# Optimization experiments

Measured on AMD Instinct MI355X. Metric: run time of the kernel, lower is better.

Reference implementation:

```python
import jax, jax.numpy as jnp
import numpy as np
from jax import lax

B, C, HH, WW = 256, 2048, 24, 8
NC = 51
KM_ITERS = 10
EPS = 1e-5


def _bn(x, g, b, m, v):
    return (x - m) / jnp.sqrt(v + EPS) * g + b


def _kmeans_ids(X):
    # X: [C, D]. Cluster the C channel vectors into 4 groups (Lloyd's, euclidean,
    # deterministic quartile init standing in for kmeans-pytorch random init).
    Cn = X.shape[0]
    centers = X[jnp.array([0, Cn // 4, Cn // 2, 3 * Cn // 4])]  # [4, D]
    xs = jnp.sum(X * X, axis=1)  # [C]

    def d2(cent):  # squared euclidean distances [C, 4]
        return xs[:, None] - 2.0 * (X @ cent.T) + jnp.sum(cent * cent, axis=1)[None]

    def step(cent, _):
        ids = jnp.argmin(d2(cent), axis=1)
        oh = jax.nn.one_hot(ids, 4, dtype=X.dtype)  # [C, 4]
        cnt = oh.sum(0)[:, None]  # [4, 1]
        new = jnp.where(cnt > 0, (oh.T @ X) / jnp.maximum(cnt, 1.0), cent)
        return new, None

    centers, _ = lax.scan(step, centers, None, length=KM_ITERS)
    return jnp.argmin(d2(centers), axis=1)  # [C]


def setup_inputs() -> dict:
    key = jax.random.key(0)
    ks = iter(jax.random.split(key, 64))
    rn = lambda shape, s=1.0: jax.random.normal(next(ks), shape, jnp.float32) * s
    ru = lambda shape: jax.random.uniform(next(ks), shape, jnp.float32, minval=0.5, maxval=1.5)
    return dict(
        x=rn((B, C, HH, WW)),
        Wg=rn((512, 2048), 0.02), bg=rn((512,), 0.02),
        g_gamma=ru((512,)), g_beta=rn((512,), 0.1), g_mean=rn((512,), 0.1), g_var=ru((512,)),
        gb_gamma=ru((512,)), gb_beta=rn((512,), 0.1), gb_mean=rn((512,), 0.1), gb_var=ru((512,)),
        Wcg=rn((NC, 512), 0.01), bcg=jnp.zeros((NC,), jnp.float32),
        W1=rn((512, 2048), 0.02), b1=rn((512,), 0.02),
        n1_gamma=ru((512,)), n1_beta=rn((512,), 0.1), n1_mean=rn((512,), 0.1), n1_var=ru((512,)),
        W2=rn((128, 512), 0.05), b2=rn((128,), 0.02),
        n2_gamma=ru((128,)), n2_beta=rn((128,), 0.1), n2_mean=rn((128,), 0.1), n2_var=ru((128,)),
        bk_gamma=ru((4, 128)), bk_beta=rn((4, 128), 0.1), bk_mean=rn((4, 128), 0.1), bk_var=ru((4, 128)),
        Wck=rn((NC, 512), 0.01), bck=jnp.zeros((NC,), jnp.float32),
    )


def reference(x, Wg, bg, g_gamma, g_beta, g_mean, g_var,
              gb_gamma, gb_beta, gb_mean, gb_var, Wcg, bcg,
              W1, b1, n1_gamma, n1_beta, n1_mean, n1_var,
              W2, b2, n2_gamma, n2_beta, n2_mean, n2_var,
              bk_gamma, bk_beta, bk_mean, bk_var, Wck, bck):
    b_, c_ = x.shape[0], x.shape[1]
    pooled = x.mean(axis=(2, 3))  # [B, C] (adaptive avgpool to 1x1)

    # ---- global branch: 1x1 conv on pooled == dense layer ----
    xg = jax.nn.relu(_bn(pooled @ Wg.T + bg, g_gamma, g_beta, g_mean, g_var))
    xg = _bn(xg, gb_gamma, gb_beta, gb_mean, gb_var)  # bottleneck_global
    x_prelogits = xg @ Wcg.T + bcg  # [B, NC]

    # ---- kmeans branch ----
    X = x.reshape(b_, c_, -1)  # per-sample [C, H*W]
    ids = jax.vmap(_kmeans_ids)(lax.stop_gradient(X))  # [B, C] int32
    masks = jax.nn.one_hot(ids, 4, dtype=x.dtype)  # [B, C, 4]
    # masking zeroes whole channels, so avgpool(masked map) == masked pooled
    Pk = jnp.einsum('bc,bck->kbc', pooled, masks)  # [4, B, C]

    # NOTE: original forward reuses norm_kmeans1 weights for all 4 branches
    h = jax.nn.relu(_bn(jnp.einsum('kbc,oc->kbo', Pk, W1) + b1,
                        n1_gamma, n1_beta, n1_mean, n1_var))  # [4, B, 512]
    h = jax.nn.relu(_bn(jnp.einsum('kbo,po->kbp', h, W2) + b2,
                        n2_gamma, n2_beta, n2_mean, n2_var))  # [4, B, 128]
    # per-branch bottleneck BN1d (stacked params [4, 128])
    h = (h - bk_mean[:, None, :]) / jnp.sqrt(bk_var[:, None, :] + EPS) \
        * bk_gamma[:, None, :] + bk_beta[:, None, :]
    # triple-nested copy loop == concat [x1|x2|x3|x4] along features
    y = jnp.transpose(h, (1, 0, 2)).reshape(b_, -1)  # [B, 512]
    y_prelogits = y @ Wck.T + bck  # [B, NC]

    return (x_prelogits, y_prelogits)
```

## Files before the change

kernel.cpp:

```cpp
#include <hip/hip_runtime.h>
#include <math.h>

#define B_   256
#define C_   2048
#define D_   192
#define EPSf 1e-5f
#define BLAS_Q 384

__device__ __forceinline__ float pw96_sq_f4(const float4* a4) {
    float r0 = 0.f, r1 = 0.f, r2 = 0.f, r3 = 0.f, r4 = 0.f, r5 = 0.f, r6 = 0.f, r7 = 0.f;
#pragma unroll
    for (int i = 0; i < 12; ++i) {
        const float4 v0 = a4[2 * i], v1 = a4[2 * i + 1];
        r0 += __fmul_rn(v0.x, v0.x); r1 += __fmul_rn(v0.y, v0.y);
        r2 += __fmul_rn(v0.z, v0.z); r3 += __fmul_rn(v0.w, v0.w);
        r4 += __fmul_rn(v1.x, v1.x); r5 += __fmul_rn(v1.y, v1.y);
        r6 += __fmul_rn(v1.z, v1.z); r7 += __fmul_rn(v1.w, v1.w);
    }
    return ((r0 + r1) + (r2 + r3)) + ((r4 + r5) + (r6 + r7));
}

__device__ __forceinline__ float pw96_sq_s(const float* a) {
    float r0 = 0.f, r1 = 0.f, r2 = 0.f, r3 = 0.f, r4 = 0.f, r5 = 0.f, r6 = 0.f, r7 = 0.f;
#pragma unroll
    for (int i = 0; i < 12; ++i) {
        r0 += __fmul_rn(a[8 * i + 0], a[8 * i + 0]);
        r1 += __fmul_rn(a[8 * i + 1], a[8 * i + 1]);
        r2 += __fmul_rn(a[8 * i + 2], a[8 * i + 2]);
        r3 += __fmul_rn(a[8 * i + 3], a[8 * i + 3]);
        r4 += __fmul_rn(a[8 * i + 4], a[8 * i + 4]);
        r5 += __fmul_rn(a[8 * i + 5], a[8 * i + 5]);
        r6 += __fmul_rn(a[8 * i + 6], a[8 * i + 6]);
        r7 += __fmul_rn(a[8 * i + 7], a[8 * i + 7]);
    }
    return ((r0 + r1) + (r2 + r3)) + ((r4 + r5) + (r6 + r7));
}

__global__ __launch_bounds__(256) void transpose_kernel(const float* __restrict__ x,
                                                        float* __restrict__ xT) {
    const int b = blockIdx.z, c0 = blockIdx.x * 64, d0 = blockIdx.y * 64;
    const float* X = x + (size_t)b * (C_ * (size_t)D_);
    float* XT      = xT + (size_t)b * (C_ * (size_t)D_);
    __shared__ float tile[64][65];
    const int tx = threadIdx.x & 63, ty = threadIdx.x >> 6;
#pragma unroll
    for (int i = 0; i < 16; ++i) {
        const int c = ty + i * 4;
        tile[c][tx] = X[(size_t)(c0 + c) * D_ + d0 + tx];
    }
    __syncthreads();
#pragma unroll
    for (int i = 0; i < 16; ++i) {
        const int d = ty + i * 4;
        XT[(size_t)(d0 + d) * C_ + c0 + tx] = tile[tx][d];
    }
}

__global__ __launch_bounds__(512) void kmeans_fast_kernel(const float* __restrict__ x,
                                                          const float* __restrict__ xT,
                                                          float* __restrict__ pooled,
                                                          unsigned char* __restrict__ ids_out) {
    const int b = blockIdx.x, t = threadIdx.x;
    const int lane = t & 63;
    const float* X   = x  + (size_t)b * (C_ * (size_t)D_);
    const float* XTb = xT + (size_t)b * (C_ * (size_t)D_);

    __shared__ __align__(16) float cent[4][192];
    __shared__ float xs_s[C_];
    __shared__ float part[6][4][192];
    __shared__ float cs4[4];
    __shared__ int   cnt[4];
    __shared__ int   changed;
    __shared__ unsigned char ids[C_];

    if (t < 192) {
        cent[0][t] = X[(size_t)0    * D_ + t];
        cent[1][t] = X[(size_t)512  * D_ + t];
        cent[2][t] = X[(size_t)1024 * D_ + t];
        cent[3][t] = X[(size_t)1536 * D_ + t];
    }

    {
        const float4* pA = (const float4*)XTb + t;
        float sq0 = 0.f, sq1 = 0.f, sq2 = 0.f, sq3 = 0.f;
        float sm0 = 0.f, sm1 = 0.f, sm2 = 0.f, sm3 = 0.f;
#pragma unroll
        for (int blk = 0; blk < 2; ++blk) {
            float q[4][8], s[4][8];
#pragma unroll
            for (int ch = 0; ch < 4; ++ch)
#pragma unroll
                for (int j = 0; j < 8; ++j) { q[ch][j] = 0.f; s[ch][j] = 0.f; }
            for (int i = 0; i < 12; ++i) {
                float4 vb[8];
#pragma unroll
                for (int u = 0; u < 8; ++u) vb[u] = pA[(blk * 96 + 8 * i + u) << 9];
#pragma unroll
                for (int u = 0; u < 8; ++u) {
                    q[0][u] += __fmul_rn(vb[u].x, vb[u].x); s[0][u] += vb[u].x;
                    q[1][u] += __fmul_rn(vb[u].y, vb[u].y); s[1][u] += vb[u].y;
                    q[2][u] += __fmul_rn(vb[u].z, vb[u].z); s[2][u] += vb[u].z;
                    q[3][u] += __fmul_rn(vb[u].w, vb[u].w); s[3][u] += vb[u].w;
                }
            }
            sq0 += ((q[0][0] + q[0][1]) + (q[0][2] + q[0][3])) + ((q[0][4] + q[0][5]) + (q[0][6] + q[0][7]));
            sq1 += ((q[1][0] + q[1][1]) + (q[1][2] + q[1][3])) + ((q[1][4] + q[1][5]) + (q[1][6] + q[1][7]));
            sq2 += ((q[2][0] + q[2][1]) + (q[2][2] + q[2][3])) + ((q[2][4] + q[2][5]) + (q[2][6] + q[2][7]));
            sq3 += ((q[3][0] + q[3][1]) + (q[3][2] + q[3][3])) + ((q[3][4] + q[3][5]) + (q[3][6] + q[3][7]));
            sm0 += ((s[0][0] + s[0][1]) + (s[0][2] + s[0][3])) + ((s[0][4] + s[0][5]) + (s[0][6] + s[0][7]));
            sm1 += ((s[1][0] + s[1][1]) + (s[1][2] + s[1][3])) + ((s[1][4] + s[1][5]) + (s[1][6] + s[1][7]));
            sm2 += ((s[2][0] + s[2][1]) + (s[2][2] + s[2][3])) + ((s[2][4] + s[2][5]) + (s[2][6] + s[2][7]));
            sm3 += ((s[3][0] + s[3][1]) + (s[3][2] + s[3][3])) + ((s[3][4] + s[3][5]) + (s[3][6] + s[3][7]));
        }
        xs_s[4 * t + 0] = sq0; xs_s[4 * t + 1] = sq1;
        xs_s[4 * t + 2] = sq2; xs_s[4 * t + 3] = sq3;
        *(float4*)(pooled + (size_t)b * C_ + 4 * t) =
            make_float4(sm0 / 192.0f, sm1 / 192.0f, sm2 / 192.0f, sm3 / 192.0f);
        ids[4 * t + 0] = 255; ids[4 * t + 1] = 255;
        ids[4 * t + 2] = 255; ids[4 * t + 3] = 255;
    }
    __syncthreads();

    for (int iter = 0;; ++iter) {
        if (t < 4) {
            cs4[t] = pw96_sq_s(cent[t]) + pw96_sq_s(cent[t] + 96);
            cnt[t] = 0;
        }
        if (t == 0) changed = 0;
        __syncthreads();

        const float q0 = cs4[0], q1 = cs4[1], q2 = cs4[2], q3 = cs4[3];

        int lc0 = 0, lc1 = 0, lc2 = 0, lc3 = 0, mych = 0;
        {
            const float4* pA = (const float4*)XTb + t;
            float acc[4][4] = {};
            for (int db = 0; db < 192; db += 8) {
                float4 vb[8];
#pragma unroll
                for (int u = 0; u < 8; ++u) vb[u] = pA[(db + u) << 9];
#pragma unroll
                for (int u = 0; u < 8; ++u) {
                    const int d = db + u;
                    const float c0 = cent[0][d], c1 = cent[1][d];
                    const float c2 = cent[2][d], c3 = cent[3][d];
                    acc[0][0] = fmaf(vb[u].x, c0, acc[0][0]);
                    acc[1][0] = fmaf(vb[u].y, c0, acc[1][0]);
                    acc[2][0] = fmaf(vb[u].z, c0, acc[2][0]);
                    acc[3][0] = fmaf(vb[u].w, c0, acc[3][0]);
                    acc[0][1] = fmaf(vb[u].x, c1, acc[0][1]);
                    acc[1][1] = fmaf(vb[u].y, c1, acc[1][1]);
                    acc[2][1] = fmaf(vb[u].z, c1, acc[2][1]);
                    acc[3][1] = fmaf(vb[u].w, c1, acc[3][1]);
                    acc[0][2] = fmaf(vb[u].x, c2, acc[0][2]);
                    acc[1][2] = fmaf(vb[u].y, c2, acc[1][2]);
                    acc[2][2] = fmaf(vb[u].z, c2, acc[2][2]);
                    acc[3][2] = fmaf(vb[u].w, c2, acc[3][2]);
                    acc[0][3] = fmaf(vb[u].x, c3, acc[0][3]);
                    acc[1][3] = fmaf(vb[u].y, c3, acc[1][3]);
                    acc[2][3] = fmaf(vb[u].z, c3, acc[2][3]);
                    acc[3][3] = fmaf(vb[u].w, c3, acc[3][3]);
                }
            }
#pragma unroll
            for (int ch = 0; ch < 4; ++ch) {
                const int c = 4 * t + ch;
                const float xv = xs_s[c];
                const float e0 = (xv - 2.0f * acc[ch][0]) + q0;
                const float e1 = (xv - 2.0f * acc[ch][1]) + q1;
                const float e2 = (xv - 2.0f * acc[ch][2]) + q2;
                const float e3 = (xv - 2.0f * acc[ch][3]) + q3;
                int id = 0; float best = e0;
                if (e1 < best) { best = e1; id = 1; }
                if (e2 < best) { best = e2; id = 2; }
                if (e3 < best) { best = e3; id = 3; }
                lc0 += (id == 0); lc1 += (id == 1); lc2 += (id == 2); lc3 += (id == 3);
                mych |= (ids[c] != (unsigned char)id);
                ids[c] = (unsigned char)id;
            }
        }
#pragma unroll
        for (int off = 32; off > 0; off >>= 1) {
            lc0 += __shfl_down(lc0, off);
            lc1 += __shfl_down(lc1, off);
            lc2 += __shfl_down(lc2, off);
            lc3 += __shfl_down(lc3, off);
        }
        if (lane == 0) {
            atomicAdd(&cnt[0], lc0); atomicAdd(&cnt[1], lc1);
            atomicAdd(&cnt[2], lc2); atomicAdd(&cnt[3], lc3);
        }
        if (mych) changed = 1;
        __syncthreads();

        if (changed == 0 || iter == 10) break;

        if (t < 288) {
            const int kb = t / 48;
            const int dg = t - kb * 48;
            const int cb = kb * BLAS_Q;
            const int ce = (cb + BLAS_Q < C_) ? (cb + BLAS_Q) : C_;
            const float4* pB = (const float4*)X + (size_t)cb * 48 + dg;
            float s[4][4] = {};
            for (int c0i = 0; c0i < ce - cb; c0i += 8) {
                float4 vb[8];
#pragma unroll
                for (int u = 0; u < 8; ++u) vb[u] = pB[(size_t)(c0i + u) * 48];
#pragma unroll
                for (int u = 0; u < 8; ++u) {
                    const int id = ids[cb + c0i + u];
                    s[0][0] += (id == 0) ? vb[u].x : 0.0f;
                    s[1][0] += (id == 0) ? vb[u].y : 0.0f;
                    s[2][0] += (id == 0) ? vb[u].z : 0.0f;
                    s[3][0] += (id == 0) ? vb[u].w : 0.0f;
                    s[0][1] += (id == 1) ? vb[u].x : 0.0f;
                    s[1][1] += (id == 1) ? vb[u].y : 0.0f;
                    s[2][1] += (id == 1) ? vb[u].z : 0.0f;
                    s[3][1] += (id == 1) ? vb[u].w : 0.0f;
                    s[0][2] += (id == 2) ? vb[u].x : 0.0f;
                    s[1][2] += (id == 2) ? vb[u].y : 0.0f;
                    s[2][2] += (id == 2) ? vb[u].z : 0.0f;
                    s[3][2] += (id == 2) ? vb[u].w : 0.0f;
                    s[0][3] += (id == 3) ? vb[u].x : 0.0f;
                    s[1][3] += (id == 3) ? vb[u].y : 0.0f;
                    s[2][3] += (id == 3) ? vb[u].z : 0.0f;
                    s[3][3] += (id == 3) ? vb[u].w : 0.0f;
                }
            }
#pragma unroll
            for (int k = 0; k < 4; ++k) {
                part[kb][k][4 * dg + 0] = s[0][k];
                part[kb][k][4 * dg + 1] = s[1][k];
                part[kb][k][4 * dg + 2] = s[2][k];
                part[kb][k][4 * dg + 3] = s[3][k];
            }
        }
        __syncthreads();
        if (t < 192) {
#pragma unroll
            for (int k = 0; k < 4; ++k) {
                float tt = part[0][k][t];
                tt += part[1][k][t];
                tt += part[2][k][t];
                tt += part[3][k][t];
                tt += part[4][k][t];
                tt += part[5][k][t];
                if (cnt[k] > 0) cent[k][t] = tt / (float)cnt[k];
            }
        }
        __syncthreads();
    }

    *(uchar4*)(ids_out + (size_t)b * C_ + 4 * t) = *(uchar4*)&ids[4 * t];
}

__global__ __launch_bounds__(256) void pool_kernel(const float* __restrict__ x,
                                                   float* __restrict__ pooled) {
    const int row  = blockIdx.x * 4 + (threadIdx.x >> 6);
    const int lane = threadIdx.x & 63;
    const float* r = x + (size_t)row * D_;
    float s = 0.f;
    if (lane < 48) {
        const float4 v = ((const float4*)r)[lane];
        s = v.x + v.y + v.z + v.w;
    }
#pragma unroll
    for (int off = 32; off > 0; off >>= 1) s += __shfl_down(s, off);
    if (lane == 0) pooled[row] = s * (1.f / 192.f);
}

__global__ __launch_bounds__(512) void kmeans_fb_kernel(const float* __restrict__ x,
                                                        unsigned char* __restrict__ ids_out) {
    const int b = blockIdx.x, t = threadIdx.x;
    const int lane = t & 63;
    const float* X = x + (size_t)b * (C_ * (size_t)D_);

    __shared__ __align__(16) float cent[4][192];
    __shared__ float xs_s[C_];
    __shared__ float cs4[4];
    __shared__ int   cnt[4];
    __shared__ int   changed;
    __shared__ unsigned char ids[C_];

    if (t < 192) {
        cent[0][t] = X[(size_t)0    * D_ + t];
        cent[1][t] = X[(size_t)512  * D_ + t];
        cent[2][t] = X[(size_t)1024 * D_ + t];
        cent[3][t] = X[(size_t)1536 * D_ + t];
    }
    for (int c = t; c < C_; c += 512) {
        const float4* r4 = (const float4*)(X + (size_t)c * D_);
        xs_s[c] = pw96_sq_f4(r4) + pw96_sq_f4(r4 + 24);
        ids[c]  = 255;
    }
    __syncthreads();

    for (int iter = 0;; ++iter) {
        if (t < 4) {
            cs4[t] = pw96_sq_s(cent[t]) + pw96_sq_s(cent[t] + 96);
            cnt[t] = 0;
        }
        if (t == 0) changed = 0;
        __syncthreads();

        const float q0 = cs4[0], q1 = cs4[1], q2 = cs4[2], q3 = cs4[3];
        int lc0 = 0, lc1 = 0, lc2 = 0, lc3 = 0, mych = 0;
        for (int j = 0; j < 4; ++j) {
            const int c = t + 512 * j;
            const float4* r4 = (const float4*)(X + (size_t)c * D_);
            float d0 = 0.f, d1 = 0.f, d2 = 0.f, d3 = 0.f;
#pragma unroll 8
            for (int i = 0; i < 48; ++i) {
                const float4 a  = r4[i];
                const float4 c0 = *(const float4*)&cent[0][4 * i];
                const float4 c1 = *(const float4*)&cent[1][4 * i];
                const float4 c2 = *(const float4*)&cent[2][4 * i];
                const float4 c3 = *(const float4*)&cent[3][4 * i];
                d0 = fmaf(a.x, c0.x, d0); d0 = fmaf(a.y, c0.y, d0);
                d0 = fmaf(a.z, c0.z, d0); d0 = fmaf(a.w, c0.w, d0);
                d1 = fmaf(a.x, c1.x, d1); d1 = fmaf(a.y, c1.y, d1);
                d1 = fmaf(a.z, c1.z, d1); d1 = fmaf(a.w, c1.w, d1);
                d2 = fmaf(a.x, c2.x, d2); d2 = fmaf(a.y, c2.y, d2);
                d2 = fmaf(a.z, c2.z, d2); d2 = fmaf(a.w, c2.w, d2);
                d3 = fmaf(a.x, c3.x, d3); d3 = fmaf(a.y, c3.y, d3);
                d3 = fmaf(a.z, c3.z, d3); d3 = fmaf(a.w, c3.w, d3);
            }
            const float xv = xs_s[c];
            const float e0 = (xv - 2.0f * d0) + q0;
            const float e1 = (xv - 2.0f * d1) + q1;
            const float e2 = (xv - 2.0f * d2) + q2;
            const float e3 = (xv - 2.0f * d3) + q3;
            int id = 0; float best = e0;
            if (e1 < best) { best = e1; id = 1; }
            if (e2 < best) { best = e2; id = 2; }
            if (e3 < best) { best = e3; id = 3; }
            lc0 += (id == 0); lc1 += (id == 1); lc2 += (id == 2); lc3 += (id == 3);
            mych |= (ids[c] != (unsigned char)id);
            ids[c] = (unsigned char)id;
        }
#pragma unroll
        for (int off = 32; off > 0; off >>= 1) {
            lc0 += __shfl_down(lc0, off);
            lc1 += __shfl_down(lc1, off);
            lc2 += __shfl_down(lc2, off);
            lc3 += __shfl_down(lc3, off);
        }
        if (lane == 0) {
            atomicAdd(&cnt[0], lc0); atomicAdd(&cnt[1], lc1);
            atomicAdd(&cnt[2], lc2); atomicAdd(&cnt[3], lc3);
        }
        if (mych) changed = 1;
        __syncthreads();

        if (changed == 0 || iter == 10) break;

        if (t < 192) {
            float t0 = 0.f, t1 = 0.f, t2 = 0.f, t3 = 0.f;
            for (int kb = 0; kb < C_; kb += BLAS_Q) {
                const int ke = (kb + BLAS_Q < C_) ? (kb + BLAS_Q) : C_;
                float s0 = 0.f, s1 = 0.f, s2 = 0.f, s3 = 0.f;
                for (int c = kb; c < ke; ++c) {
                    const float xv = X[(size_t)c * D_ + t];
                    const int id = ids[c];
                    s0 += (id == 0) ? xv : 0.0f;
                    s1 += (id == 1) ? xv : 0.0f;
                    s2 += (id == 2) ? xv : 0.0f;
                    s3 += (id == 3) ? xv : 0.0f;
                }
                t0 += s0; t1 += s1; t2 += s2; t3 += s3;
            }
            if (cnt[0] > 0) cent[0][t] = t0 / (float)cnt[0];
            if (cnt[1] > 0) cent[1][t] = t1 / (float)cnt[1];
            if (cnt[2] > 0) cent[2][t] = t2 / (float)cnt[2];
            if (cnt[3] > 0) cent[3][t] = t3 / (float)cnt[3];
        }
        __syncthreads();
    }

    for (int c = t; c < C_; c += 512) ids_out[(size_t)b * C_ + c] = ids[c];
}

__device__ __forceinline__ float bn_apply(float v, float g, float be, float m, float va) {
    return (v - m) / sqrtf(va + EPSf) * g + be;
}

__global__ __launch_bounds__(256) void gemm1_kernel(
    const float* __restrict__ pooled, const unsigned char* __restrict__ ids,
    const float* __restrict__ Wg, const float* __restrict__ bg,
    const float* __restrict__ g_gamma, const float* __restrict__ g_beta,
    const float* __restrict__ g_mean, const float* __restrict__ g_var,
    const float* __restrict__ gb_gamma, const float* __restrict__ gb_beta,
    const float* __restrict__ gb_mean, const float* __restrict__ gb_var,
    const float* __restrict__ W1, const float* __restrict__ b1,
    const float* __restrict__ n1_gamma, const float* __restrict__ n1_beta,
    const float* __restrict__ n1_mean, const float* __restrict__ n1_var,
    float* __restrict__ xg2, float* __restrict__ h1) {
    const int z = blockIdx.z;
    const int bn0 = blockIdx.x * 64, bm0 = blockIdx.y * 64;
    const float* Bmat = (z == 0) ? Wg : W1;
    __shared__ float As[32][68];
    __shared__ float Bs[32][68];
    float acc[4][4] = {};
    const int t = threadIdx.x;
    const int tx = t & 15, ty = t >> 4;

    for (int k0 = 0; k0 < 2048; k0 += 32) {
#pragma unroll
        for (int u = 0; u < 2; ++u) {
            const int idx = t + 256 * u;
            const int m = idx >> 3, kc = idx & 7;
            float4 v = *(const float4*)(pooled + (size_t)(bm0 + m) * 2048 + k0 + kc * 4);
            if (z > 0) {
                const unsigned int uu =
                    *(const unsigned int*)(ids + (size_t)(bm0 + m) * 2048 + k0 + kc * 4);
                const unsigned int k = (unsigned int)(z - 1);
                v.x = ((uu & 0xffu) == k) ? v.x : 0.f;
                v.y = (((uu >> 8) & 0xffu) == k) ? v.y : 0.f;
                v.z = (((uu >> 16) & 0xffu) == k) ? v.z : 0.f;
                v.w = (((uu >> 24) & 0xffu) == k) ? v.w : 0.f;
            }
            As[kc * 4 + 0][m] = v.x; As[kc * 4 + 1][m] = v.y;
            As[kc * 4 + 2][m] = v.z; As[kc * 4 + 3][m] = v.w;
            const float4 wv = *(const float4*)(Bmat + (size_t)(bn0 + m) * 2048 + k0 + kc * 4);
            Bs[kc * 4 + 0][m] = wv.x; Bs[kc * 4 + 1][m] = wv.y;
            Bs[kc * 4 + 2][m] = wv.z; Bs[kc * 4 + 3][m] = wv.w;
        }
        __syncthreads();
#pragma unroll 8
        for (int kk = 0; kk < 32; ++kk) {
            const float4 a = *(const float4*)&As[kk][ty * 4];
            const float4 wv = *(const float4*)&Bs[kk][tx * 4];
            const float av[4] = {a.x, a.y, a.z, a.w};
            const float bv[4] = {wv.x, wv.y, wv.z, wv.w};
#pragma unroll
            for (int i = 0; i < 4; ++i)
#pragma unroll
                for (int j = 0; j < 4; ++j) acc[i][j] += av[i] * bv[j];
        }
        __syncthreads();
    }

    const int m0 = bm0 + ty * 4, n0 = bn0 + tx * 4;
    if (z == 0) {
#pragma unroll
        for (int j = 0; j < 4; ++j) {
            const int n = n0 + j;
            const float bgv = bg[n];
            const float g1 = g_gamma[n], be1 = g_beta[n], mm1 = g_mean[n], vv1 = g_var[n];
            const float g2 = gb_gamma[n], be2 = gb_beta[n], mm2 = gb_mean[n], vv2 = gb_var[n];
#pragma unroll
            for (int i = 0; i < 4; ++i) {
                float v = acc[i][j] + bgv;
                v = bn_apply(v, g1, be1, mm1, vv1);
                v = fmaxf(v, 0.f);
                v = bn_apply(v, g2, be2, mm2, vv2);
                xg2[(size_t)(m0 + i) * 512 + n] = v;
            }
        }
    } else {
        const int k = z - 1;
#pragma unroll
        for (int j = 0; j < 4; ++j) {
            const int n = n0 + j;
            const float b1v = b1[n];
            const float g1 = n1_gamma[n], be1 = n1_beta[n], mm1 = n1_mean[n], vv1 = n1_var[n];
#pragma unroll
            for (int i = 0; i < 4; ++i) {
                float v = acc[i][j] + b1v;
                v = bn_apply(v, g1, be1, mm1, vv1);
                v = fmaxf(v, 0.f);
                h1[((size_t)k * 256 + (m0 + i)) * 512 + n] = v;
            }
        }
    }
}

__global__ __launch_bounds__(256) void gemm2_kernel(
    const float* __restrict__ h1, const float* __restrict__ W2,
    const float* __restrict__ b2,
    const float* __restrict__ n2_gamma, const float* __restrict__ n2_beta,
    const float* __restrict__ n2_mean, const float* __restrict__ n2_var,
    const float* __restrict__ bk_gamma, const float* __restrict__ bk_beta,
    const float* __restrict__ bk_mean, const float* __restrict__ bk_var,
    float* __restrict__ yv) {
    const int bn0 = blockIdx.x * 64, bm0 = blockIdx.y * 64;
    __shared__ float As[32][68];
    __shared__ float Bs[32][68];
    float acc[4][4] = {};
    const int t = threadIdx.x;
    const int tx = t & 15, ty = t >> 4;

    for (int k0 = 0; k0 < 512; k0 += 32) {
#pragma unroll
        for (int u = 0; u < 2; ++u) {
            const int idx = t + 256 * u;
            const int m = idx >> 3, kc = idx & 7;
            const float4 v = *(const float4*)(h1 + (size_t)(bm0 + m) * 512 + k0 + kc * 4);
            As[kc * 4 + 0][m] = v.x; As[kc * 4 + 1][m] = v.y;
            As[kc * 4 + 2][m] = v.z; As[kc * 4 + 3][m] = v.w;
            const float4 wv = *(const float4*)(W2 + (size_t)(bn0 + m) * 512 + k0 + kc * 4);
            Bs[kc * 4 + 0][m] = wv.x; Bs[kc * 4 + 1][m] = wv.y;
            Bs[kc * 4 + 2][m] = wv.z; Bs[kc * 4 + 3][m] = wv.w;
        }
        __syncthreads();
#pragma unroll 8
        for (int kk = 0; kk < 32; ++kk) {
            const float4 a = *(const float4*)&As[kk][ty * 4];
            const float4 wv = *(const float4*)&Bs[kk][tx * 4];
            const float av[4] = {a.x, a.y, a.z, a.w};
            const float bv[4] = {wv.x, wv.y, wv.z, wv.w};
#pragma unroll
            for (int i = 0; i < 4; ++i)
#pragma unroll
                for (int j = 0; j < 4; ++j) acc[i][j] += av[i] * bv[j];
        }
        __syncthreads();
    }

    const int m0 = bm0 + ty * 4, n0 = bn0 + tx * 4;
#pragma unroll
    for (int j = 0; j < 4; ++j) {
        const int n = n0 + j;
        const float b2v = b2[n];
        const float g1 = n2_gamma[n], be1 = n2_beta[n], mm1 = n2_mean[n], vv1 = n2_var[n];
#pragma unroll
        for (int i = 0; i < 4; ++i) {
            const int row = m0 + i;
            const int k = row >> 8, b = row & 255;
            float v = acc[i][j] + b2v;
            v = bn_apply(v, g1, be1, mm1, vv1);
            v = fmaxf(v, 0.f);
            const int pi = k * 128 + n;
            v = bn_apply(v, bk_gamma[pi], bk_beta[pi], bk_mean[pi], bk_var[pi]);
            yv[(size_t)b * 512 + pi] = v;
        }
    }
}

__global__ __launch_bounds__(128) void head_kernel(
    const float* __restrict__ xg2, const float* __restrict__ yv,
    const float* __restrict__ Wcg, const float* __restrict__ bcg,
    const float* __restrict__ Wck, const float* __restrict__ bck,
    float* __restrict__ out) {
    const int b = blockIdx.x, t = threadIdx.x;
    __shared__ float xr[512], yr[512];
    ((float4*)xr)[t] = ((const float4*)(xg2 + (size_t)b * 512))[t];
    ((float4*)yr)[t] = ((const float4*)(yv + (size_t)b * 512))[t];
    __syncthreads();
    if (t < 51) {
        float acc = 0.f;
        const float4* wr = (const float4*)(Wcg + (size_t)t * 512);
        const float4* xv = (const float4*)xr;
#pragma unroll 8
        for (int p = 0; p < 128; ++p) {
            const float4 w4 = wr[p], v4 = xv[p];
            acc += w4.x * v4.x + w4.y * v4.y + w4.z * v4.z + w4.w * v4.w;
        }
        out[(size_t)b * 51 + t] = acc + bcg[t];
    } else if (t >= 64 && t < 115) {
        const int n = t - 64;
        float acc = 0.f;
        const float4* wr = (const float4*)(Wck + (size_t)n * 512);
        const float4* yv4 = (const float4*)yr;
#pragma unroll 8
        for (int p = 0; p < 128; ++p) {
            const float4 w4 = wr[p], v4 = yv4[p];
            acc += w4.x * v4.x + w4.y * v4.y + w4.z * v4.z + w4.w * v4.w;
        }
        out[(size_t)(B_ * 51) + (size_t)b * 51 + n] = acc + bck[n];
    }
}

extern "C" void kernel_launch(void* const* d_in, const int* in_sizes, int n_in,
                              void* d_out, int out_size, void* d_ws, size_t ws_size,
                              hipStream_t stream) {
    const float* x        = (const float*)d_in[0];
    const float* Wg       = (const float*)d_in[1];
    const float* bg       = (const float*)d_in[2];
    const float* g_gamma  = (const float*)d_in[3];
    const float* g_beta   = (const float*)d_in[4];
    const float* g_mean   = (const float*)d_in[5];
    const float* g_var    = (const float*)d_in[6];
    const float* gb_gamma = (const float*)d_in[7];
    const float* gb_beta  = (const float*)d_in[8];
    const float* gb_mean  = (const float*)d_in[9];
    const float* gb_var   = (const float*)d_in[10];
    const float* Wcg      = (const float*)d_in[11];
    const float* bcg      = (const float*)d_in[12];
    const float* W1       = (const float*)d_in[13];
    const float* b1       = (const float*)d_in[14];
    const float* n1_gamma = (const float*)d_in[15];
    const float* n1_beta  = (const float*)d_in[16];
    const float* n1_mean  = (const float*)d_in[17];
    const float* n1_var   = (const float*)d_in[18];
    const float* W2       = (const float*)d_in[19];
    const float* b2       = (const float*)d_in[20];
    const float* n2_gamma = (const float*)d_in[21];
    const float* n2_beta  = (const float*)d_in[22];
    const float* n2_mean  = (const float*)d_in[23];
    const float* n2_var   = (const float*)d_in[24];
    const float* bk_gamma = (const float*)d_in[25];
    const float* bk_beta  = (const float*)d_in[26];
    const float* bk_mean  = (const float*)d_in[27];
    const float* bk_var   = (const float*)d_in[28];
    const float* Wck      = (const float*)d_in[29];
    const float* bck      = (const float*)d_in[30];
    float* out = (float*)d_out;

    const size_t xt_elems    = (size_t)B_ * C_ * D_;
    const size_t small_elems = 524288 + 131072 + 524288 + 131072;
    const size_t need_fast   = xt_elems * 4 + small_elems * 4 + 524288 + 256;

    if (ws_size >= need_fast) {
        float* xT          = (float*)d_ws;
        float* pooled      = xT + xt_elems;
        unsigned char* ids = (unsigned char*)(pooled + 524288);
        float* xg2         = (float*)(ids + 524288);
        float* h1          = xg2 + 131072;
        float* yv          = h1 + 524288;

        transpose_kernel<<<dim3(32, 3, B_), dim3(256), 0, stream>>>(x, xT);
        kmeans_fast_kernel<<<dim3(B_), dim3(512), 0, stream>>>(x, xT, pooled, ids);
        gemm1_kernel<<<dim3(8, 4, 5), dim3(256), 0, stream>>>(
            pooled, ids, Wg, bg, g_gamma, g_beta, g_mean, g_var,
            gb_gamma, gb_beta, gb_mean, gb_var, W1, b1,
            n1_gamma, n1_beta, n1_mean, n1_var, xg2, h1);
        gemm2_kernel<<<dim3(2, 16), dim3(256), 0, stream>>>(
            h1, W2, b2, n2_gamma, n2_beta, n2_mean, n2_var,
            bk_gamma, bk_beta, bk_mean, bk_var, yv);
        head_kernel<<<dim3(B_), dim3(128), 0, stream>>>(xg2, yv, Wcg, bcg, Wck, bck, out);
    } else {
        float* pooled      = (float*)d_ws;
        unsigned char* ids = (unsigned char*)(pooled + 524288);
        float* xg2         = (float*)(ids + 524288);
        float* h1          = xg2 + 131072;
        float* yv          = h1 + 524288;

        pool_kernel<<<dim3((B_ * C_) / 4), dim3(256), 0, stream>>>(x, pooled);
        kmeans_fb_kernel<<<dim3(B_), dim3(512), 0, stream>>>(x, ids);
        gemm1_kernel<<<dim3(8, 4, 5), dim3(256), 0, stream>>>(
            pooled, ids, Wg, bg, g_gamma, g_beta, g_mean, g_var,
            gb_gamma, gb_beta, gb_mean, gb_var, W1, b1,
            n1_gamma, n1_beta, n1_mean, n1_var, xg2, h1);
        gemm2_kernel<<<dim3(2, 16), dim3(256), 0, stream>>>(
            h1, W2, b2, n2_gamma, n2_beta, n2_mean, n2_var,
            bk_gamma, bk_beta, bk_mean, bk_var, yv);
        head_kernel<<<dim3(B_), dim3(128), 0, stream>>>(xg2, yv, Wcg, bcg, Wck, bck, out);
    }
}
```

Measured before the change: 1.791 ms.

## Fuse pooling and norms into transpose, double kmeans block to 1024 threads

The transpose kernel now loads a full 64-channel row tile into LDS, computes per-channel squared norms and pooled means there, and writes the transposed data. This removes the separate norm/pool pass from the kmeans kernel. The kmeans kernel moves to 1024 threads with two channels per thread and float2 loads, double-buffered in both the distance and centroid-accumulation phases, to raise parallelism and hide memory latency. The cost is more LDS in the transpose (64x193 floats, lowering its occupancy), an extra xs buffer in global memory, and fewer registers available per thread at 1024 threads.

```diff
diff --git a/kernel.cpp b/kernel.cpp
--- a/kernel.cpp
+++ b/kernel.cpp
@@ -36,30 +36,92 @@
     return ((r0 + r1) + (r2 + r3)) + ((r4 + r5) + (r6 + r7));
 }
 
+__device__ __forceinline__ float pw96_sum_s(const float* a) {
+    float r0 = 0.f, r1 = 0.f, r2 = 0.f, r3 = 0.f, r4 = 0.f, r5 = 0.f, r6 = 0.f, r7 = 0.f;
+#pragma unroll
+    for (int i = 0; i < 12; ++i) {
+        r0 += a[8 * i + 0]; r1 += a[8 * i + 1];
+        r2 += a[8 * i + 2]; r3 += a[8 * i + 3];
+        r4 += a[8 * i + 4]; r5 += a[8 * i + 5];
+        r6 += a[8 * i + 6]; r7 += a[8 * i + 7];
+    }
+    return ((r0 + r1) + (r2 + r3)) + ((r4 + r5) + (r6 + r7));
+}
+
 __global__ __launch_bounds__(256) void transpose_kernel(const float* __restrict__ x,
-                                                        float* __restrict__ xT) {
-    const int b = blockIdx.z, c0 = blockIdx.x * 64, d0 = blockIdx.y * 64;
+                                                        float* __restrict__ xT,
+                                                        float* __restrict__ pooled,
+                                                        float* __restrict__ xs_g) {
+    const int c0 = blockIdx.x * 64, b = blockIdx.y;
     const float* X = x + (size_t)b * (C_ * (size_t)D_);
     float* XT      = xT + (size_t)b * (C_ * (size_t)D_);
-    __shared__ float tile[64][65];
-    const int tx = threadIdx.x & 63, ty = threadIdx.x >> 6;
-#pragma unroll
-    for (int i = 0; i < 16; ++i) {
-        const int c = ty + i * 4;
-        tile[c][tx] = X[(size_t)(c0 + c) * D_ + d0 + tx];
+    __shared__ float lds[64 * 193];
+    const int t = threadIdx.x;
+
+#pragma unroll
+    for (int i = 0; i < 12; ++i) {
+        const int idx = i * 256 + t;
+        const int r = idx / 48, j = idx % 48;
+        const float4 v = *(const float4*)(X + (size_t)(c0 + r) * D_ + 4 * j);
+        float* p = &lds[r * 193 + 4 * j];
+        p[0] = v.x; p[1] = v.y; p[2] = v.z; p[3] = v.w;
     }
     __syncthreads();
-#pragma unroll
-    for (int i = 0; i < 16; ++i) {
-        const int d = ty + i * 4;
-        XT[(size_t)(d0 + d) * C_ + c0 + tx] = tile[tx][d];
-    }
-}
-
-__global__ __launch_bounds__(512) void kmeans_fast_kernel(const float* __restrict__ x,
-                                                          const float* __restrict__ xT,
-                                                          float* __restrict__ pooled,
-                                                          unsigned char* __restrict__ ids_out) {
+
+    if (t < 64) {
+        const float* row = &lds[t * 193];
+        xs_g[(size_t)b * C_ + c0 + t]   = pw96_sq_s(row)  + pw96_sq_s(row + 96);
+        pooled[(size_t)b * C_ + c0 + t] = (pw96_sum_s(row) + pw96_sum_s(row + 96)) / 192.0f;
+    }
+
+#pragma unroll
+    for (int i = 0; i < 48; ++i) {
+        const int idx = i * 256 + t;
+        const int d = idx >> 6, ch = idx & 63;
+        XT[(size_t)d * C_ + c0 + ch] = lds[ch * 193 + d];
+    }
+}
+
+__device__ __forceinline__ void pa_comp8_f2(const float2 (&vb)[8], int dbase,
+                                            const float (*cent)[192],
+                                            float (&acc)[2][4]) {
+#pragma unroll
+    for (int u = 0; u < 8; ++u) {
+        const int d = dbase + u;
+        const float c0 = cent[0][d], c1 = cent[1][d];
+        const float c2 = cent[2][d], c3 = cent[3][d];
+        acc[0][0] = fmaf(vb[u].x, c0, acc[0][0]);
+        acc[1][0] = fmaf(vb[u].y, c0, acc[1][0]);
+        acc[0][1] = fmaf(vb[u].x, c1, acc[0][1]);
+        acc[1][1] = fmaf(vb[u].y, c1, acc[1][1]);
+        acc[0][2] = fmaf(vb[u].x, c2, acc[0][2]);
+        acc[1][2] = fmaf(vb[u].y, c2, acc[1][2]);
+        acc[0][3] = fmaf(vb[u].x, c3, acc[0][3]);
+        acc[1][3] = fmaf(vb[u].y, c3, acc[1][3]);
+    }
+}
+
+__device__ __forceinline__ void pb_comp8_f2(const float2 (&vb)[8], int cbase,
+                                            const unsigned char* ids,
+                                            float (&s)[2][4]) {
+#pragma unroll
+    for (int u = 0; u < 8; ++u) {
+        const int id = ids[cbase + u];
+        s[0][0] += (id == 0) ? vb[u].x : 0.0f;
+        s[1][0] += (id == 0) ? vb[u].y : 0.0f;
+        s[0][1] += (id == 1) ? vb[u].x : 0.0f;
+        s[1][1] += (id == 1) ? vb[u].y : 0.0f;
+        s[0][2] += (id == 2) ? vb[u].x : 0.0f;
+        s[1][2] += (id == 2) ? vb[u].y : 0.0f;
+        s[0][3] += (id == 3) ? vb[u].x : 0.0f;
+        s[1][3] += (id == 3) ? vb[u].y : 0.0f;
+    }
+}
+
+__global__ __launch_bounds__(1024) void kmeans_fast_kernel(const float* __restrict__ x,
+                                                           const float* __restrict__ xT,
+                                                           const float* __restrict__ xs_g,
+                                                           unsigned char* __restrict__ ids_out) {
     const int b = blockIdx.x, t = threadIdx.x;
     const int lane = t & 63;
     const float* X   = x  + (size_t)b * (C_ * (size_t)D_);
@@ -79,45 +141,11 @@
         cent[2][t] = X[(size_t)1024 * D_ + t];
         cent[3][t] = X[(size_t)1536 * D_ + t];
     }
-
     {
-        const float4* pA = (const float4*)XTb + t;
-        float sq0 = 0.f, sq1 = 0.f, sq2 = 0.f, sq3 = 0.f;
-        float sm0 = 0.f, sm1 = 0.f, sm2 = 0.f, sm3 = 0.f;
-#pragma unroll
-        for (int blk = 0; blk < 2; ++blk) {
-            float q[4][8], s[4][8];
-#pragma unroll
-            for (int ch = 0; ch < 4; ++ch)
-#pragma unroll
-                for (int j = 0; j < 8; ++j) { q[ch][j] = 0.f; s[ch][j] = 0.f; }
-            for (int i = 0; i < 12; ++i) {
-                float4 vb[8];
-#pragma unroll
-                for (int u = 0; u < 8; ++u) vb[u] = pA[(blk * 96 + 8 * i + u) << 9];
-#pragma unroll
-                for (int u = 0; u < 8; ++u) {
-                    q[0][u] += __fmul_rn(vb[u].x, vb[u].x); s[0][u] += vb[u].x;
-                    q[1][u] += __fmul_rn(vb[u].y, vb[u].y); s[1][u] += vb[u].y;
-                    q[2][u] += __fmul_rn(vb[u].z, vb[u].z); s[2][u] += vb[u].z;
-                    q[3][u] += __fmul_rn(vb[u].w, vb[u].w); s[3][u] += vb[u].w;
-                }
-            }
-            sq0 += ((q[0][0] + q[0][1]) + (q[0][2] + q[0][3])) + ((q[0][4] + q[0][5]) + (q[0][6] + q[0][7]));
-            sq1 += ((q[1][0] + q[1][1]) + (q[1][2] + q[1][3])) + ((q[1][4] + q[1][5]) + (q[1][6] + q[1][7]));
-            sq2 += ((q[2][0] + q[2][1]) + (q[2][2] + q[2][3])) + ((q[2][4] + q[2][5]) + (q[2][6] + q[2][7]));
-            sq3 += ((q[3][0] + q[3][1]) + (q[3][2] + q[3][3])) + ((q[3][4] + q[3][5]) + (q[3][6] + q[3][7]));
-            sm0 += ((s[0][0] + s[0][1]) + (s[0][2] + s[0][3])) + ((s[0][4] + s[0][5]) + (s[0][6] + s[0][7]));
-            sm1 += ((s[1][0] + s[1][1]) + (s[1][2] + s[1][3])) + ((s[1][4] + s[1][5]) + (s[1][6] + s[1][7]));
-            sm2 += ((s[2][0] + s[2][1]) + (s[2][2] + s[2][3])) + ((s[2][4] + s[2][5]) + (s[2][6] + s[2][7]));
-            sm3 += ((s[3][0] + s[3][1]) + (s[3][2] + s[3][3])) + ((s[3][4] + s[3][5]) + (s[3][6] + s[3][7]));
-        }
-        xs_s[4 * t + 0] = sq0; xs_s[4 * t + 1] = sq1;
-        xs_s[4 * t + 2] = sq2; xs_s[4 * t + 3] = sq3;
-        *(float4*)(pooled + (size_t)b * C_ + 4 * t) =
-            make_float4(sm0 / 192.0f, sm1 / 192.0f, sm2 / 192.0f, sm3 / 192.0f);
-        ids[4 * t + 0] = 255; ids[4 * t + 1] = 255;
-        ids[4 * t + 2] = 255; ids[4 * t + 3] = 255;
+        const int c2 = 2 * t;
+        const float2 xv2 = *(const float2*)(xs_g + (size_t)b * C_ + c2);
+        xs_s[c2] = xv2.x; xs_s[c2 + 1] = xv2.y;
+        ids[c2] = 255; ids[c2 + 1] = 255;
     }
     __syncthreads();
 
@@ -133,38 +161,24 @@
 
         int lc0 = 0, lc1 = 0, lc2 = 0, lc3 = 0, mych = 0;
         {
-            const float4* pA = (const float4*)XTb + t;
-            float acc[4][4] = {};
-            for (int db = 0; db < 192; db += 8) {
-                float4 vb[8];
-#pragma unroll
-                for (int u = 0; u < 8; ++u) vb[u] = pA[(db + u) << 9];
-#pragma unroll
-                for (int u = 0; u < 8; ++u) {
-                    const int d = db + u;
-                    const float c0 = cent[0][d], c1 = cent[1][d];
-                    const float c2 = cent[2][d], c3 = cent[3][d];
-                    acc[0][0] = fmaf(vb[u].x, c0, acc[0][0]);
-                    acc[1][0] = fmaf(vb[u].y, c0, acc[1][0]);
-                    acc[2][0] = fmaf(vb[u].z, c0, acc[2][0]);
-                    acc[3][0] = fmaf(vb[u].w, c0, acc[3][0]);
-                    acc[0][1] = fmaf(vb[u].x, c1, acc[0][1]);
-                    acc[1][1] = fmaf(vb[u].y, c1, acc[1][1]);
-                    acc[2][1] = fmaf(vb[u].z, c1, acc[2][1]);
-                    acc[3][1] = fmaf(vb[u].w, c1, acc[3][1]);
-                    acc[0][2] = fmaf(vb[u].x, c2, acc[0][2]);
-                    acc[1][2] = fmaf(vb[u].y, c2, acc[1][2]);
-                    acc[2][2] = fmaf(vb[u].z, c2, acc[2][2]);
-                    acc[3][2] = fmaf(vb[u].w, c2, acc[3][2]);
-                    acc[0][3] = fmaf(vb[u].x, c3, acc[0][3]);
-                    acc[1][3] = fmaf(vb[u].y, c3, acc[1][3]);
-                    acc[2][3] = fmaf(vb[u].z, c3, acc[2][3]);
-                    acc[3][3] = fmaf(vb[u].w, c3, acc[3][3]);
+            const float2* pA = (const float2*)XTb + t;
+            float acc[2][4] = {};
+            float2 bufA[8], bufB[8];
+#pragma unroll
+            for (int u = 0; u < 8; ++u) bufA[u] = pA[(size_t)u << 10];
+            for (int db = 0; db < 192; db += 16) {
+#pragma unroll
+                for (int u = 0; u < 8; ++u) bufB[u] = pA[(size_t)(db + 8 + u) << 10];
+                pa_comp8_f2(bufA, db, cent, acc);
+                if (db + 16 < 192) {
+#pragma unroll
+                    for (int u = 0; u < 8; ++u) bufA[u] = pA[(size_t)(db + 16 + u) << 10];
                 }
-            }
-#pragma unroll
-            for (int ch = 0; ch < 4; ++ch) {
-                const int c = 4 * t + ch;
+                pa_comp8_f2(bufB, db + 8, cent, acc);
+            }
+#pragma unroll
+            for (int ch = 0; ch < 2; ++ch) {
+                const int c = 2 * t + ch;
                 const float xv = xs_s[c];
                 const float e0 = (xv - 2.0f * acc[ch][0]) + q0;
                 const float e1 = (xv - 2.0f * acc[ch][1]) + q1;
@@ -195,44 +209,31 @@
 
         if (changed == 0 || iter == 10) break;
 
-        if (t < 288) {
-            const int kb = t / 48;
-            const int dg = t - kb * 48;
+        if (t < 576) {
+            const int kb = t / 96;
+            const int dg = t - kb * 96;
             const int cb = kb * BLAS_Q;
             const int ce = (cb + BLAS_Q < C_) ? (cb + BLAS_Q) : C_;
-            const float4* pB = (const float4*)X + (size_t)cb * 48 + dg;
-            float s[4][4] = {};
-            for (int c0i = 0; c0i < ce - cb; c0i += 8) {
-                float4 vb[8];
-#pragma unroll
-                for (int u = 0; u < 8; ++u) vb[u] = pB[(size_t)(c0i + u) * 48];
-#pragma unroll
-                for (int u = 0; u < 8; ++u) {
-                    const int id = ids[cb + c0i + u];
-                    s[0][0] += (id == 0) ? vb[u].x : 0.0f;
-                    s[1][0] += (id == 0) ? vb[u].y : 0.0f;
-                    s[2][0] += (id == 0) ? vb[u].z : 0.0f;
-                    s[3][0] += (id == 0) ? vb[u].w : 0.0f;
-                    s[0][1] += (id == 1) ? vb[u].x : 0.0f;
-                    s[1][1] += (id == 1) ? vb[u].y : 0.0f;
-                    s[2][1] += (id == 1) ? vb[u].z : 0.0f;
-                    s[3][1] += (id == 1) ? vb[u].w : 0.0f;
-                    s[0][2] += (id == 2) ? vb[u].x : 0.0f;
-                    s[1][2] += (id == 2) ? vb[u].y : 0.0f;
-                    s[2][2] += (id == 2) ? vb[u].z : 0.0f;
-                    s[3][2] += (id == 2) ? vb[u].w : 0.0f;
-                    s[0][3] += (id == 3) ? vb[u].x : 0.0f;
-                    s[1][3] += (id == 3) ? vb[u].y : 0.0f;
-                    s[2][3] += (id == 3) ? vb[u].z : 0.0f;
-                    s[3][3] += (id == 3) ? vb[u].w : 0.0f;
+            const int nb = (ce - cb) >> 3;
+            const float2* pB = (const float2*)X + (size_t)cb * 96 + dg;
+            float s[2][4] = {};
+            float2 bufA[8], bufB[8];
+#pragma unroll
+            for (int u = 0; u < 8; ++u) bufA[u] = pB[(size_t)u * 96];
+            for (int ib = 0; ib < nb; ib += 2) {
+#pragma unroll
+                for (int u = 0; u < 8; ++u) bufB[u] = pB[(size_t)((ib + 1) * 8 + u) * 96];
+                pb_comp8_f2(bufA, cb + ib * 8, ids, s);
+                if (ib + 2 < nb) {
+#pragma unroll
+                    for (int u = 0; u < 8; ++u) bufA[u] = pB[(size_t)((ib + 2) * 8 + u) * 96];
                 }
+                pb_comp8_f2(bufB, cb + (ib + 1) * 8, ids, s);
             }
 #pragma unroll
             for (int k = 0; k < 4; ++k) {
-                part[kb][k][4 * dg + 0] = s[0][k];
-                part[kb][k][4 * dg + 1] = s[1][k];
-                part[kb][k][4 * dg + 2] = s[2][k];
-                part[kb][k][4 * dg + 3] = s[3][k];
+                part[kb][k][2 * dg + 0] = s[0][k];
+                part[kb][k][2 * dg + 1] = s[1][k];
             }
         }
         __syncthreads();
@@ -251,7 +252,7 @@
         __syncthreads();
     }
 
-    *(uchar4*)(ids_out + (size_t)b * C_ + 4 * t) = *(uchar4*)&ids[4 * t];
+    *(uchar2*)(ids_out + (size_t)b * C_ + 2 * t) = *(uchar2*)&ids[2 * t];
 }
 
 __global__ __launch_bounds__(256) void pool_kernel(const float* __restrict__ x,
@@ -608,19 +609,20 @@
     float* out = (float*)d_out;
 
     const size_t xt_elems    = (size_t)B_ * C_ * D_;
-    const size_t small_elems = 524288 + 131072 + 524288 + 131072;
+    const size_t small_elems = 524288 * 2 + 131072 + 524288 + 131072;
     const size_t need_fast   = xt_elems * 4 + small_elems * 4 + 524288 + 256;
 
     if (ws_size >= need_fast) {
         float* xT          = (float*)d_ws;
         float* pooled      = xT + xt_elems;
-        unsigned char* ids = (unsigned char*)(pooled + 524288);
+        float* xs_g        = pooled + 524288;
+        unsigned char* ids = (unsigned char*)(xs_g + 524288);
         float* xg2         = (float*)(ids + 524288);
         float* h1          = xg2 + 131072;
         float* yv          = h1 + 524288;
 
-        transpose_kernel<<<dim3(32, 3, B_), dim3(256), 0, stream>>>(x, xT);
-        kmeans_fast_kernel<<<dim3(B_), dim3(512), 0, stream>>>(x, xT, pooled, ids);
+        transpose_kernel<<<dim3(32, B_), dim3(256), 0, stream>>>(x, xT, pooled, xs_g);
+        kmeans_fast_kernel<<<dim3(B_), dim3(1024), 0, stream>>>(x, xT, xs_g, ids);
         gemm1_kernel<<<dim3(8, 4, 5), dim3(256), 0, stream>>>(
             pooled, ids, Wg, bg, g_gamma, g_beta, g_mean, g_var,
             gb_gamma, gb_beta, gb_mean, gb_var, W1, b1,
```

New measurement: 1.749 ms. 2.4% less time.
